# Kernel tuning notes

Measured on AMD Instinct MI355X. Metric: run time of the kernel, lower is better.

Reference implementation:

```python
import jax, jax.numpy as jnp
import numpy as np

EMB = 256   # EMB_SIZE hard-coded in source
H = 8       # num heads (all heads share the same Q/K/V, as in source)
DK = EMB // H  # 32
B, T = 16, 2048
LN_EPS = 1e-5


def _layernorm(a, g, b):
    m = jnp.mean(a, axis=-1, keepdims=True)
    v = jnp.mean(jnp.square(a - m), axis=-1, keepdims=True)
    return (a - m) * jax.lax.rsqrt(v + LN_EPS) * g + b


def setup_inputs() -> dict:
    key = jax.random.key(0)
    ks = jax.random.split(key, 8)
    sc = 0.02
    return {
        "x": jax.random.normal(ks[0], (B, T, EMB), jnp.float32),
        "Wq": jax.random.normal(ks[1], (EMB, DK), jnp.float32) * sc,
        "Wk": jax.random.normal(ks[2], (EMB, DK), jnp.float32) * sc,
        "Wv": jax.random.normal(ks[3], (EMB, DK), jnp.float32) * sc,
        "Wp": jax.random.normal(ks[4], (EMB, EMB), jnp.float32) * sc,
        "bp": jnp.zeros((EMB,), jnp.float32),
        "W1": jax.random.normal(ks[5], (EMB, 4 * EMB), jnp.float32) * sc,
        "b1": jnp.zeros((4 * EMB,), jnp.float32),
        "W2": jax.random.normal(ks[6], (4 * EMB, EMB), jnp.float32) * sc,
        "b2": jnp.zeros((EMB,), jnp.float32),
        "g1": jnp.ones((EMB,), jnp.float32),
        "be1": jnp.zeros((EMB,), jnp.float32),
        "g2": jnp.ones((EMB,), jnp.float32),
        "be2": jnp.zeros((EMB,), jnp.float32),
    }


def reference(x, Wq, Wk, Wv, Wp, bp, W1, b1, W2, b2, g1, be1, g2, be2):
    # Single shared-head QKV projections (bias-free), as in source
    q = x @ Wq  # [B,T,DK]
    k = x @ Wk
    v = x @ Wv
    # Causal self-attention with explicit score matrix [B,T,T]
    scores = jnp.einsum("btd,bsd->bts", q, k) / jnp.sqrt(jnp.float32(DK))
    causal = jnp.tril(jnp.ones((T, T), dtype=bool))
    scores = jnp.where(causal, scores, -jnp.inf)
    a = jax.nn.softmax(scores, axis=-1)
    attn = jnp.einsum("bts,bsd->btd", a, v)  # [B,T,DK]
    # Source concatenates h identical copies of the same attention output
    cat = jnp.tile(attn, (1, 1, H))  # [B,T,EMB]
    mh = cat @ Wp + bp
    y1 = _layernorm(x + mh, g1, be1)
    ff = jax.nn.gelu(y1 @ W1 + b1, approximate=False) @ W2 + b2
    return _layernorm(y1 + ff, g2, be2)
```

## Files before the change

### kernel.cpp

```cpp
#include <hip/hip_runtime.h>

#define BB 16
#define TT 2048
#define EE 256
#define DK 32
#define MM (BB*TT)
#define FF 1024

typedef __bf16 bf16_t;
typedef __bf16 bf16x8 __attribute__((ext_vector_type(8)));
typedef __bf16 bf16x4 __attribute__((ext_vector_type(4)));
typedef float  f32x4  __attribute__((ext_vector_type(4)));

__device__ __forceinline__ f32x4 mfma16(bf16x8 a, bf16x8 b, f32x4 c){
  return __builtin_amdgcn_mfma_f32_16x16x32_bf16(a, b, c, 0, 0, 0);
}
__device__ __forceinline__ void gload_lds16(const void* g, void* l){
  __builtin_amdgcn_global_load_lds((__attribute__((address_space(1))) void*)g,
                                   (__attribute__((address_space(3))) void*)l,
                                   16, 0, 0);
}

__launch_bounds__(256)
__global__ void prep_kernel(const float* __restrict__ Wq, const float* __restrict__ Wk,
                            const float* __restrict__ Wv, const float* __restrict__ Wp,
                            const float* __restrict__ W1, const float* __restrict__ W2,
                            bf16_t* __restrict__ wqkv, float* __restrict__ wpe,
                            bf16_t* __restrict__ w1t, bf16_t* __restrict__ w2t)
{
  const int i = blockIdx.x*256 + threadIdx.x;
  if (i < 96*256) {
    const int r = i >> 8, c = i & 255;
    float v;
    if (r < 32)      v = Wq[c*32 + r] * 0.17677669529663687f;
    else if (r < 64) v = Wk[c*32 + (r-32)];
    else             v = Wv[c*32 + (r-64)];
    wqkv[i] = (bf16_t)v;
  }
  if (i < 32*256) {
    const int d = i >> 8, n = i & 255;
    float s = 0.f;
    #pragma unroll
    for (int h = 0; h < 8; ++h) s += Wp[(h*32 + d)*256 + n];
    wpe[i] = s;
  }
  if (i < 1024*256) {
    const int n = i >> 8, k = i & 255;
    w1t[i] = (bf16_t)W1[(size_t)k*1024 + n];
  }
  if (i < 256*1024) {
    const int n = i >> 10, k = i & 1023;
    w2t[i] = (bf16_t)W2[(size_t)k*256 + n];
  }
}

__launch_bounds__(256)
__global__ void qkv_kernel(const float* __restrict__ x, const bf16_t* __restrict__ wqkv,
                           bf16_t* __restrict__ q, bf16_t* __restrict__ kd,
                           bf16_t* __restrict__ vT)
{
  __shared__ bf16_t Ws[96*256];
  bf16_t* Vt = Ws;
  const int tid = threadIdx.x;
  #pragma unroll
  for (int i = 0; i < 12; ++i) {
    const int v8  = tid + i*256;
    const int row = v8 >> 5;
    const int bir = (v8 & 31) * 16;
    *(bf16x8*)((char*)Ws + row*512 + (bir ^ ((row & 7) << 4))) =
        *(const bf16x8*)(wqkv + (size_t)v8*8);
  }
  __syncthreads();

  const int w = tid >> 6, l = tid & 63;
  const int lr = l & 15, lk4 = l >> 4, lkb = lk4*8;
  const int m0 = blockIdx.x * 64;
  const int arow = m0 + w*16 + lr;
  const float* xr = x + (size_t)arow * 256;

  f32x4 acc[6] = {};
  #pragma unroll
  for (int s = 0; s < 8; ++s) {
    const int kb = s*32 + lkb;
    const float4 v0 = *(const float4*)(xr + kb);
    const float4 v1 = *(const float4*)(xr + kb + 4);
    bf16x8 a;
    a[0]=(bf16_t)v0.x; a[1]=(bf16_t)v0.y; a[2]=(bf16_t)v0.z; a[3]=(bf16_t)v0.w;
    a[4]=(bf16_t)v1.x; a[5]=(bf16_t)v1.y; a[6]=(bf16_t)v1.z; a[7]=(bf16_t)v1.w;
    #pragma unroll
    for (int j = 0; j < 6; ++j) {
      const int nrow = j*16 + lr;
      const bf16x8 bf = *(const bf16x8*)((const char*)Ws + nrow*512 +
                                         ((kb*2) ^ ((nrow & 7) << 4)));
      acc[j] = mfma16(a, bf, acc[j]);
    }
  }
  #pragma unroll
  for (int j = 0; j < 4; ++j) {
    #pragma unroll
    for (int r = 0; r < 4; ++r) {
      const int orow = m0 + w*16 + lk4*4 + r;
      const int col  = j*16 + lr;
      const bf16_t v = (bf16_t)acc[j][r];
      if (col < 32) q[(size_t)orow*32 + col] = v;
      else          kd[(size_t)orow*32 + (col-32)] = v;
    }
  }
  __syncthreads();
  #pragma unroll
  for (int j = 4; j < 6; ++j)
    #pragma unroll
    for (int r = 0; r < 4; ++r) {
      const int d = (j-4)*16 + lr;
      const int t = w*16 + lk4*4 + r;
      *(bf16_t*)((char*)Vt + d*128 + ((((t>>3) ^ (d&7))<<4) | ((t&7)*2))) =
          (bf16_t)acc[j][r];
    }
  __syncthreads();
  {
    const int d = tid >> 3, c8 = tid & 7;
    const bf16x8 v = *(const bf16x8*)((char*)Vt + d*128 + ((c8 ^ (d&7))<<4));
    *(bf16x8*)(vT + ((size_t)(m0 >> 11)*32 + d)*TT + (m0 & 2047) + c8*8) = v;
  }
}

__launch_bounds__(256)
__global__ void attnp_kernel(const bf16_t* __restrict__ q, const bf16_t* __restrict__ kd,
                             const bf16_t* __restrict__ vT,
                             float* __restrict__ part_acc, float* __restrict__ part_ml)
{
  __shared__ bf16_t P[4][16*128];
  const int tid = threadIdx.x;
  const int w = tid >> 6, l = tid & 63;
  const int wv = blockIdx.x*4 + w;
  const int lr = l & 15, g4 = l >> 4;
  const float NEG_INF = -__builtin_inff();

  const int b = wv / 320;
  const int u = wv - b*320;
  int r, base;
  if      (u >= 192) { r = 3; base = 192; }
  else if (u >= 96)  { r = 2; base = 96;  }
  else if (u >= 32)  { r = 1; base = 32;  }
  else               { r = 0; base = 0;   }
  const int qq = u - base;
  const int g  = r*32 + qq / (r+1);
  const int c  = qq - (qq / (r+1))*(r+1);
  const int t_total = (g >> 3) + 1;
  const int t0 = c*4;
  const int t1 = min(t0 + 4, t_total);

  const bf16_t* qb = q  + (size_t)b*TT*32;
  const bf16_t* kb = kd + (size_t)b*TT*32;
  const bf16_t* vb = vT + (size_t)b*32*TT;
  const int q0 = g*16;
  const int qg = q0 + lr;

  const bf16x8 qa = *(const bf16x8*)(qb + (size_t)(q0 + lr)*32 + g4*8);
  const bf16_t* v0r = vb + (size_t)lr*TT;
  const bf16_t* v1r = vb + (size_t)(16 + lr)*TT;

  f32x4 acc0 = {0.f,0.f,0.f,0.f}, acc1 = {0.f,0.f,0.f,0.f};
  float mrun = NEG_INF, lsum = 0.f;
  char* pb = (char*)&P[w][0];
  const int swz = (lr & 7) << 4;
  const f32x4 zf = {0.f,0.f,0.f,0.f};

  for (int t = t0; t < t1; ++t) {
    const int k0 = t * 128;
    f32x4 s[8];
    #pragma unroll
    for (int cc = 0; cc < 8; ++cc) {
      const bf16x8 kf = *(const bf16x8*)(kb + (size_t)(k0 + cc*16 + lr)*32 + g4*8);
      s[cc] = mfma16(kf, qa, zf);
    }
    if (t == t_total - 1) {
      #pragma unroll
      for (int cc = 0; cc < 8; ++cc)
        #pragma unroll
        for (int rr = 0; rr < 4; ++rr)
          if (k0 + cc*16 + g4*4 + rr > qg) s[cc][rr] = NEG_INF;
    }
    float mt = NEG_INF;
    #pragma unroll
    for (int cc = 0; cc < 8; ++cc) {
      float a01 = fmaxf(s[cc][0], s[cc][1]), a23 = fmaxf(s[cc][2], s[cc][3]);
      mt = fmaxf(mt, fmaxf(a01, a23));
    }
    mt = fmaxf(mt, __shfl_xor(mt, 16));
    mt = fmaxf(mt, __shfl_xor(mt, 32));
    const float mn = fmaxf(mrun, mt);
    const float sc = __expf(mrun - mn);
    float ps = 0.f;
    #pragma unroll
    for (int cc = 0; cc < 8; ++cc) {
      float p0 = __expf(s[cc][0]-mn), p1 = __expf(s[cc][1]-mn);
      float p2 = __expf(s[cc][2]-mn), p3 = __expf(s[cc][3]-mn);
      s[cc][0]=p0; s[cc][1]=p1; s[cc][2]=p2; s[cc][3]=p3;
      ps += (p0+p1) + (p2+p3);
    }
    ps += __shfl_xor(ps, 16);
    ps += __shfl_xor(ps, 32);
    lsum = lsum*sc + ps;
    mrun = mn;
    acc0 *= sc; acc1 *= sc;
    #pragma unroll
    for (int cc = 0; cc < 8; ++cc) {
      bf16x4 pk;
      pk[0]=(bf16_t)s[cc][0]; pk[1]=(bf16_t)s[cc][1];
      pk[2]=(bf16_t)s[cc][2]; pk[3]=(bf16_t)s[cc][3];
      *(bf16x4*)(pb + lr*256 + ((cc*32 + g4*8) ^ swz)) = pk;
    }
    #pragma unroll
    for (int h = 0; h < 4; ++h) {
      const bf16x8 pbf = *(const bf16x8*)(pb + lr*256 + ((h*64 + g4*16) ^ swz));
      acc0 = mfma16(*(const bf16x8*)(v0r + k0 + h*32 + g4*8), pbf, acc0);
      acc1 = mfma16(*(const bf16x8*)(v1r + k0 + h*32 + g4*8), pbf, acc1);
    }
  }
  float* pa = part_acc + (size_t)wv*512;
  *(f32x4*)(pa + l*8)     = acc0;
  *(f32x4*)(pa + l*8 + 4) = acc1;
  if (l < 16) {
    part_ml[wv*32 + l]      = mrun;
    part_ml[wv*32 + 16 + l] = lsum;
  }
}

__launch_bounds__(256)
__global__ void attnc_kernel(const float* __restrict__ part_acc,
                             const float* __restrict__ part_ml,
                             bf16_t* __restrict__ attn)
{
  const int tid = threadIdx.x;
  const int id = blockIdx.x*4 + (tid >> 6);
  const int l = tid & 63, lr = l & 15, g4 = l >> 4;
  const int b = id >> 7, g = id & 127;
  const int r = g >> 5;
  const int base = (r == 0) ? 0 : (r == 1) ? 32 : (r == 2) ? 96 : 192;
  const int p0 = b*320 + base + (g - (r << 5))*(r + 1);
  const int nc = r + 1;
  const float NEG_INF = -__builtin_inff();

  float m0v=NEG_INF,m1v=NEG_INF,m2v=NEG_INF,m3v=NEG_INF;
  float l0v=0,l1v=0,l2v=0,l3v=0;
  f32x4 a00={0,0,0,0},a01={0,0,0,0},a10={0,0,0,0},a11={0,0,0,0};
  f32x4 a20={0,0,0,0},a21={0,0,0,0},a30={0,0,0,0},a31={0,0,0,0};
  {
    const float* pa = part_acc + (size_t)p0*512;
    a00 = *(const f32x4*)(pa + l*8); a01 = *(const f32x4*)(pa + l*8 + 4);
    m0v = part_ml[p0*32 + lr]; l0v = part_ml[p0*32 + 16 + lr];
  }
  if (nc > 1) {
    const float* pa = part_acc + (size_t)(p0+1)*512;
    a10 = *(const f32x4*)(pa + l*8); a11 = *(const f32x4*)(pa + l*8 + 4);
    m1v = part_ml[(p0+1)*32 + lr]; l1v = part_ml[(p0+1)*32 + 16 + lr];
  }
  if (nc > 2) {
    const float* pa = part_acc + (size_t)(p0+2)*512;
    a20 = *(const f32x4*)(pa + l*8); a21 = *(const f32x4*)(pa + l*8 + 4);
    m2v = part_ml[(p0+2)*32 + lr]; l2v = part_ml[(p0+2)*32 + 16 + lr];
  }
  if (nc > 3) {
    const float* pa = part_acc + (size_t)(p0+3)*512;
    a30 = *(const f32x4*)(pa + l*8); a31 = *(const f32x4*)(pa + l*8 + 4);
    m3v = part_ml[(p0+3)*32 + lr]; l3v = part_ml[(p0+3)*32 + 16 + lr];
  }
  const float M = fmaxf(fmaxf(m0v, m1v), fmaxf(m2v, m3v));
  const float w0 = __expf(m0v - M), w1 = __expf(m1v - M);
  const float w2 = __expf(m2v - M), w3 = __expf(m3v - M);
  const float L = l0v*w0 + l1v*w1 + l2v*w2 + l3v*w3;
  const float inv = 1.0f / L;
  f32x4 o0 = (a00*w0 + a10*w1 + a20*w2 + a30*w3) * inv;
  f32x4 o1 = (a01*w0 + a11*w1 + a21*w2 + a31*w3) * inv;

  bf16_t* ao = attn + ((size_t)b*TT + g*16 + lr)*32;
  bf16x4 ob0, ob1;
  ob0[0]=(bf16_t)o0[0]; ob0[1]=(bf16_t)o0[1]; ob0[2]=(bf16_t)o0[2]; ob0[3]=(bf16_t)o0[3];
  ob1[0]=(bf16_t)o1[0]; ob1[1]=(bf16_t)o1[1]; ob1[2]=(bf16_t)o1[2]; ob1[3]=(bf16_t)o1[3];
  *(bf16x4*)(ao + g4*4)      = ob0;
  *(bf16x4*)(ao + 16 + g4*4) = ob1;
}

__launch_bounds__(256)
__global__ void ln1_kernel(const float* __restrict__ x, const bf16_t* __restrict__ attn,
                           const float* __restrict__ wpe, const float* __restrict__ bp,
                           const float* __restrict__ g1, const float* __restrict__ be1,
                           bf16_t* __restrict__ y1b)
{
  __shared__ float Wp_s[32*256];
  const int tid = threadIdx.x;
  for (int i = tid; i < 32*64; i += 256)
    ((float4*)Wp_s)[i] = ((const float4*)wpe)[i];
  __syncthreads();

  const int w = tid >> 6, l = tid & 63;
  const int n = l * 4;
  const float4 gv  = *(const float4*)(g1  + n);
  const float4 bev = *(const float4*)(be1 + n);
  const float4 bpv = *(const float4*)(bp  + n);

  #pragma unroll 1
  for (int it = 0; it < 8; ++it) {
    const int row = blockIdx.x*32 + it*4 + w;
    const bf16_t* ar = attn + (size_t)row*32;
    float a[32];
    #pragma unroll
    for (int i = 0; i < 4; ++i) {
      const bf16x8 t = *(const bf16x8*)(ar + i*8);
      #pragma unroll
      for (int j = 0; j < 8; ++j) a[i*8 + j] = (float)t[j];
    }
    float mh[4] = {bpv.x, bpv.y, bpv.z, bpv.w};
    #pragma unroll
    for (int d = 0; d < 32; ++d) {
      const float4 wv = *(const float4*)(Wp_s + d*256 + n);
      const float ad = a[d];
      mh[0] = fmaf(ad, wv.x, mh[0]); mh[1] = fmaf(ad, wv.y, mh[1]);
      mh[2] = fmaf(ad, wv.z, mh[2]); mh[3] = fmaf(ad, wv.w, mh[3]);
    }
    const float4 xv = *(const float4*)(x + (size_t)row*256 + n);
    const float t0 = xv.x + mh[0], t1 = xv.y + mh[1];
    const float t2 = xv.z + mh[2], t3 = xv.w + mh[3];
    float s1 = (t0+t1) + (t2+t3);
    float s2 = (t0*t0 + t1*t1) + (t2*t2 + t3*t3);
    #pragma unroll
    for (int m = 1; m < 64; m <<= 1) { s1 += __shfl_xor(s1, m); s2 += __shfl_xor(s2, m); }
    const float mean = s1 * (1.0f/256.0f);
    const float var  = s2 * (1.0f/256.0f) - mean*mean;
    const float rs   = rsqrtf(var + 1e-5f);
    float4 yv;
    yv.x = (t0-mean)*rs*gv.x + bev.x; yv.y = (t1-mean)*rs*gv.y + bev.y;
    yv.z = (t2-mean)*rs*gv.z + bev.z; yv.w = (t3-mean)*rs*gv.w + bev.w;
    bf16x4 yb; yb[0]=(bf16_t)yv.x; yb[1]=(bf16_t)yv.y; yb[2]=(bf16_t)yv.z; yb[3]=(bf16_t)yv.w;
    *(bf16x4*)(y1b + (size_t)row*256 + n) = yb;
  }
}

__launch_bounds__(256)
__global__ void ff1_kernel(const bf16_t* __restrict__ A, const bf16_t* __restrict__ Bt,
                           const float* __restrict__ b1, bf16_t* __restrict__ H)
{
  __shared__ char SM[32768];
  char* As = SM;
  char* Bs = SM + 16384;
  const int tid = threadIdx.x;
  const int w = tid >> 6, l = tid & 63;
  const int m0 = blockIdx.x * 128, n0 = blockIdx.y * 128;
  const int wm = (w >> 1) * 64, wn = (w & 1) * 64;
  const int lr = l & 15, lk4 = l >> 4;
  const int srow = l >> 3;
  const int scol = ((l & 7) ^ srow) * 8;
  const bf16_t* Ab = A  + (size_t)m0*256 + scol;
  const bf16_t* Bb = Bt + (size_t)n0*256 + scol;

  f32x4 acc[4][4] = {};

  for (int t = 0; t < 4; ++t) {
    const int k0 = t*64;
    #pragma unroll
    for (int i_ = 0; i_ < 4; ++i_) {
      const int r0_ = w*32 + i_*8;
      gload_lds16(Ab + (size_t)(r0_ + srow)*256 + k0, As + r0_*128);
      gload_lds16(Bb + (size_t)(r0_ + srow)*256 + k0, Bs + r0_*128);
    }
    __syncthreads();
    #pragma unroll
    for (int kk = 0; kk < 2; ++kk) {
      bf16x8 af[4], bf[4];
      #pragma unroll
      for (int i = 0; i < 4; ++i) {
        const int row = wm + i*16 + lr;
        af[i] = *(const bf16x8*)(As + row*128 +
                                 ((kk*64 + lk4*16) ^ ((row & 7) << 4)));
      }
      #pragma unroll
      for (int j = 0; j < 4; ++j) {
        const int row = wn + j*16 + lr;
        bf[j] = *(const bf16x8*)(Bs + row*128 +
                                 ((kk*64 + lk4*16) ^ ((row & 7) << 4)));
      }
      #pragma unroll
      for (int i = 0; i < 4; ++i)
        #pragma unroll
        for (int j = 0; j < 4; ++j)
          acc[i][j] = mfma16(af[i], bf[j], acc[i][j]);
    }
    __syncthreads();
  }

  #pragma unroll
  for (int i = 0; i < 4; ++i)
    #pragma unroll
    for (int j = 0; j < 4; ++j) {
      const int col = wn + j*16 + lr;
      const float bias = b1[n0 + col];
      #pragma unroll
      for (int r = 0; r < 4; ++r) {
        const int row = wm + i*16 + lk4*4 + r;
        const float v = acc[i][j][r] + bias;
        const float z = 1.5957691216057308f * v * fmaf(0.044715f, v*v, 1.0f);
        const float gg = v * __builtin_amdgcn_rcpf(1.0f + __expf(-z));
        *(bf16_t*)(SM + row*256 + ((((col>>3) ^ (row&7))<<4) | ((col&7)*2))) =
            (bf16_t)gg;
      }
    }
  __syncthreads();
  #pragma unroll
  for (int p = 0; p < 8; ++p) {
    const int idx = p*256 + tid;
    const int row = idx >> 4, c8 = idx & 15;
    const bf16x8 v = *(const bf16x8*)(SM + row*256 + ((c8 ^ (row&7))<<4));
    *(bf16x8*)(H + (size_t)(m0 + row)*FF + n0 + c8*8) = v;
  }
}

__launch_bounds__(512)
__global__ void ff2_kernel(const bf16_t* __restrict__ A, const bf16_t* __restrict__ Bt,
                           const float* __restrict__ b2, const bf16_t* __restrict__ y1b,
                           const float* __restrict__ g2, const float* __restrict__ be2,
                           float* __restrict__ out)
{
  __shared__ bf16_t As[64*64];
  __shared__ bf16_t Bs[256*64];
  __shared__ float red[64*8];
  const int tid = threadIdx.x;
  const int w = tid >> 6, l = tid & 63;
  const int m0 = blockIdx.x * 64;
  const int wm = (w >> 2) * 32, wn = (w & 3) * 64;
  const int lr = l & 15, lk4 = l >> 4;
  const int srow = l >> 3;
  const int scol = ((l & 7) ^ srow) * 8;
  const bf16_t* Ab = A + (size_t)m0*FF + scol;
  const bf16_t* Bb = Bt + scol;

  f32x4 acc[2][4] = {};

  for (int t = 0; t < 16; ++t) {
    const int k0 = t*64;
    {
      const int r0_ = w*8;
      gload_lds16(Ab + (size_t)(r0_ + srow)*FF + k0, (char*)As + r0_*128);
    }
    #pragma unroll
    for (int i_ = 0; i_ < 4; ++i_) {
      const int r0_ = w*32 + i_*8;
      gload_lds16(Bb + (size_t)(r0_ + srow)*FF + k0, (char*)Bs + r0_*128);
    }
    __syncthreads();
    #pragma unroll
    for (int kk = 0; kk < 2; ++kk) {
      bf16x8 af[2], bf[4];
      #pragma unroll
      for (int i = 0; i < 2; ++i) {
        const int row = wm + i*16 + lr;
        af[i] = *(const bf16x8*)((const char*)As + row*128 +
                                 ((kk*64 + lk4*16) ^ ((row & 7) << 4)));
      }
      #pragma unroll
      for (int j = 0; j < 4; ++j) {
        const int row = wn + j*16 + lr;
        bf[j] = *(const bf16x8*)((const char*)Bs + row*128 +
                                 ((kk*64 + lk4*16) ^ ((row & 7) << 4)));
      }
      #pragma unroll
      for (int i = 0; i < 2; ++i)
        #pragma unroll
        for (int j = 0; j < 4; ++j)
          acc[i][j] = mfma16(af[i], bf[j], acc[i][j]);
    }
    __syncthreads();
  }

  #pragma unroll
  for (int i = 0; i < 2; ++i)
    #pragma unroll
    for (int j = 0; j < 4; ++j) {
      const int col = wn + j*16 + lr;
      #pragma unroll
      for (int r = 0; r < 4; ++r) {
        const int row = m0 + wm + i*16 + lk4*4 + r;
        acc[i][j][r] += b2[col] + (float)y1b[(size_t)row*256 + col];
      }
    }
  #pragma unroll
  for (int i = 0; i < 2; ++i)
    #pragma unroll
    for (int r = 0; r < 4; ++r) {
      float s1 = (acc[i][0][r] + acc[i][1][r]) + (acc[i][2][r] + acc[i][3][r]);
      float s2 = (acc[i][0][r]*acc[i][0][r] + acc[i][1][r]*acc[i][1][r]) +
                 (acc[i][2][r]*acc[i][2][r] + acc[i][3][r]*acc[i][3][r]);
      #pragma unroll
      for (int m = 1; m < 16; m <<= 1) { s1 += __shfl_xor(s1, m); s2 += __shfl_xor(s2, m); }
      if (lr == 0) {
        const int rl = wm + i*16 + lk4*4 + r;
        red[rl*8 + (w & 3)*2]     = s1;
        red[rl*8 + (w & 3)*2 + 1] = s2;
      }
    }
  __syncthreads();
  #pragma unroll
  for (int i = 0; i < 2; ++i)
    #pragma unroll
    for (int r = 0; r < 4; ++r) {
      const int rl = wm + i*16 + lk4*4 + r;
      const float S1 = (red[rl*8+0] + red[rl*8+2]) + (red[rl*8+4] + red[rl*8+6]);
      const float S2 = (red[rl*8+1] + red[rl*8+3]) + (red[rl*8+5] + red[rl*8+7]);
      const float mean = S1 * (1.0f/256.0f);
      const float var  = S2 * (1.0f/256.0f) - mean*mean;
      const float rs   = rsqrtf(var + 1e-5f);
      #pragma unroll
      for (int j = 0; j < 4; ++j) {
        const int col = wn + j*16 + lr;
        out[(size_t)(m0 + rl)*256 + col] = (acc[i][j][r] - mean)*rs*g2[col] + be2[col];
      }
    }
}

extern "C" void kernel_launch(void* const* d_in, const int* in_sizes, int n_in,
                              void* d_out, int out_size, void* d_ws, size_t ws_size,
                              hipStream_t stream)
{
  const float* x   = (const float*)d_in[0];
  const float* Wq  = (const float*)d_in[1];
  const float* Wk  = (const float*)d_in[2];
  const float* Wv  = (const float*)d_in[3];
  const float* Wp  = (const float*)d_in[4];
  const float* bp  = (const float*)d_in[5];
  const float* W1  = (const float*)d_in[6];
  const float* b1  = (const float*)d_in[7];
  const float* W2  = (const float*)d_in[8];
  const float* b2  = (const float*)d_in[9];
  const float* g1  = (const float*)d_in[10];
  const float* be1 = (const float*)d_in[11];
  const float* g2  = (const float*)d_in[12];
  const float* be2 = (const float*)d_in[13];

  char* ws = (char*)d_ws;
  bf16_t* qd   = (bf16_t*)(ws + ((size_t)0  << 20));
  bf16_t* kd   = (bf16_t*)(ws + ((size_t)2  << 20));
  bf16_t* vTd  = (bf16_t*)(ws + ((size_t)4  << 20));
  bf16_t* attn = (bf16_t*)(ws + ((size_t)6  << 20));
  bf16_t* y1b  = (bf16_t*)(ws + ((size_t)8  << 20));
  bf16_t* h1   = (bf16_t*)(ws + ((size_t)24 << 20));
  bf16_t* wqkv = (bf16_t*)(ws + ((size_t)88 << 20));
  float*  wpe  = (float*) (ws + ((size_t)89 << 20));
  bf16_t* w1t  = (bf16_t*)(ws + ((size_t)90 << 20));
  bf16_t* w2t  = (bf16_t*)(ws + ((size_t)91 << 20));
  float*  pml  = (float*) (ws + ((size_t)92 << 20));
  float*  pacc = (float*) (ws + ((size_t)93 << 20));
  float* out = (float*)d_out;

  prep_kernel<<<1024, 256, 0, stream>>>(Wq, Wk, Wv, Wp, W1, W2, wqkv, wpe, w1t, w2t);
  qkv_kernel<<<512, 256, 0, stream>>>(x, wqkv, qd, kd, vTd);
  attnp_kernel<<<1280, 256, 0, stream>>>(qd, kd, vTd, pacc, pml);
  attnc_kernel<<<512, 256, 0, stream>>>(pacc, pml, attn);
  ln1_kernel<<<1024, 256, 0, stream>>>(x, attn, wpe, bp, g1, be1, y1b);
  ff1_kernel<<<dim3(256, 8), 256, 0, stream>>>(y1b, w1t, b1, h1);
  ff2_kernel<<<512, 512, 0, stream>>>(h1, w2t, b2, y1b, g2, be2, out);
}
```

Measured before the change: 147.0 us.

## Double-buffer LDS tiles in FFN GEMM kernels with async global-to-LDS prefetch

Both FFN GEMM kernels (ff1 and ff2) now keep two LDS stages and issue the global-to-LDS loads for tile t+2 while tile t is being computed. Explicit vmcnt waits and raw s_barrier calls replace __syncthreads, and s_setprio raises wave priority during the MFMA section. Bias, gamma and beta values are hoisted into registers before the loop. The cost is more LDS per block (64KB for ff1, 80KB for ff2), which can lower occupancy, and the hand-tuned vmcnt counts must match the number of loads issued per stage.

```diff
diff --git a/kernel.cpp b/kernel.cpp
--- a/kernel.cpp
+++ b/kernel.cpp
@@ -341,9 +341,7 @@
 __global__ void ff1_kernel(const bf16_t* __restrict__ A, const bf16_t* __restrict__ Bt,
                            const float* __restrict__ b1, bf16_t* __restrict__ H)
 {
-  __shared__ char SM[32768];
-  char* As = SM;
-  char* Bs = SM + 16384;
+  __shared__ char SM[65536];
   const int tid = threadIdx.x;
   const int w = tid >> 6, l = tid & 63;
   const int m0 = blockIdx.x * 128, n0 = blockIdx.y * 128;
@@ -354,31 +352,49 @@
   const bf16_t* Ab = A  + (size_t)m0*256 + scol;
   const bf16_t* Bb = Bt + (size_t)n0*256 + scol;
 
+  float bias[4];
+  #pragma unroll
+  for (int j = 0; j < 4; ++j) bias[j] = b1[n0 + wn + j*16 + lr];
+  asm volatile("s_waitcnt vmcnt(0)" ::: "memory");
+  __builtin_amdgcn_sched_barrier(0);
+
+  #define FF1_ST(t, d)                                                        \
+    { const int k0_ = (t)*64;                                                 \
+      _Pragma("unroll")                                                       \
+      for (int i_ = 0; i_ < 4; ++i_) {                                        \
+        const int r0_ = w*32 + i_*8;                                          \
+        gload_lds16(Ab + (size_t)(r0_ + srow)*256 + k0_,                      \
+                    SM + (d)*16384 + r0_*128);                                \
+        gload_lds16(Bb + (size_t)(r0_ + srow)*256 + k0_,                      \
+                    SM + 32768 + (d)*16384 + r0_*128);                        \
+      } }
+
+  FF1_ST(0, 0);
+  FF1_ST(1, 1);
+
   f32x4 acc[4][4] = {};
-
+  #pragma unroll
   for (int t = 0; t < 4; ++t) {
-    const int k0 = t*64;
-    #pragma unroll
-    for (int i_ = 0; i_ < 4; ++i_) {
-      const int r0_ = w*32 + i_*8;
-      gload_lds16(Ab + (size_t)(r0_ + srow)*256 + k0, As + r0_*128);
-      gload_lds16(Bb + (size_t)(r0_ + srow)*256 + k0, Bs + r0_*128);
-    }
-    __syncthreads();
+    if (t < 3) { asm volatile("s_waitcnt vmcnt(8)" ::: "memory"); }
+    else       { asm volatile("s_waitcnt vmcnt(0)" ::: "memory"); }
+    __builtin_amdgcn_sched_barrier(0);
+    __builtin_amdgcn_s_barrier();
+    __builtin_amdgcn_sched_barrier(0);
+    const char* as = SM + (t&1)*16384;
+    const char* bs = SM + 32768 + (t&1)*16384;
+    __builtin_amdgcn_s_setprio(1);
     #pragma unroll
     for (int kk = 0; kk < 2; ++kk) {
       bf16x8 af[4], bf[4];
       #pragma unroll
       for (int i = 0; i < 4; ++i) {
         const int row = wm + i*16 + lr;
-        af[i] = *(const bf16x8*)(As + row*128 +
-                                 ((kk*64 + lk4*16) ^ ((row & 7) << 4)));
+        af[i] = *(const bf16x8*)(as + row*128 + ((kk*64 + lk4*16) ^ ((row & 7) << 4)));
       }
       #pragma unroll
       for (int j = 0; j < 4; ++j) {
         const int row = wn + j*16 + lr;
-        bf[j] = *(const bf16x8*)(Bs + row*128 +
-                                 ((kk*64 + lk4*16) ^ ((row & 7) << 4)));
+        bf[j] = *(const bf16x8*)(bs + row*128 + ((kk*64 + lk4*16) ^ ((row & 7) << 4)));
       }
       #pragma unroll
       for (int i = 0; i < 4; ++i)
@@ -386,19 +402,22 @@
         for (int j = 0; j < 4; ++j)
           acc[i][j] = mfma16(af[i], bf[j], acc[i][j]);
     }
-    __syncthreads();
-  }
+    __builtin_amdgcn_s_setprio(0);
+    __builtin_amdgcn_s_barrier();
+    __builtin_amdgcn_sched_barrier(0);
+    if (t + 2 < 4) FF1_ST(t+2, t&1);
+  }
+  #undef FF1_ST
 
   #pragma unroll
   for (int i = 0; i < 4; ++i)
     #pragma unroll
     for (int j = 0; j < 4; ++j) {
       const int col = wn + j*16 + lr;
-      const float bias = b1[n0 + col];
       #pragma unroll
       for (int r = 0; r < 4; ++r) {
         const int row = wm + i*16 + lk4*4 + r;
-        const float v = acc[i][j][r] + bias;
+        const float v = acc[i][j][r] + bias[j];
         const float z = 1.5957691216057308f * v * fmaf(0.044715f, v*v, 1.0f);
         const float gg = v * __builtin_amdgcn_rcpf(1.0f + __expf(-z));
         *(bf16_t*)(SM + row*256 + ((((col>>3) ^ (row&7))<<4) | ((col&7)*2))) =
@@ -421,9 +440,7 @@
                            const float* __restrict__ g2, const float* __restrict__ be2,
                            float* __restrict__ out)
 {
-  __shared__ bf16_t As[64*64];
-  __shared__ bf16_t Bs[256*64];
-  __shared__ float red[64*8];
+  __shared__ char SM[81920];
   const int tid = threadIdx.x;
   const int w = tid >> 6, l = tid & 63;
   const int m0 = blockIdx.x * 64;
@@ -434,34 +451,52 @@
   const bf16_t* Ab = A + (size_t)m0*FF + scol;
   const bf16_t* Bb = Bt + scol;
 
+  float b2r[4], g2r[4], be2r[4];
+  #pragma unroll
+  for (int j = 0; j < 4; ++j) {
+    const int col = wn + j*16 + lr;
+    b2r[j] = b2[col]; g2r[j] = g2[col]; be2r[j] = be2[col];
+  }
+  asm volatile("s_waitcnt vmcnt(0)" ::: "memory");
+  __builtin_amdgcn_sched_barrier(0);
+
+  #define FF2_ST(t, d)                                                        \
+    { const int k0_ = (t)*64;                                                 \
+      gload_lds16(Ab + (size_t)(w*8 + srow)*FF + k0_,                         \
+                  SM + (d)*8192 + (w*8)*128);                                 \
+      _Pragma("unroll")                                                       \
+      for (int i_ = 0; i_ < 4; ++i_) {                                        \
+        const int r0_ = w*32 + i_*8;                                          \
+        gload_lds16(Bb + (size_t)(r0_ + srow)*FF + k0_,                       \
+                    SM + 16384 + (d)*32768 + r0_*128);                        \
+      } }
+
+  FF2_ST(0, 0);
+  FF2_ST(1, 1);
+
   f32x4 acc[2][4] = {};
-
+  #pragma unroll 1
   for (int t = 0; t < 16; ++t) {
-    const int k0 = t*64;
-    {
-      const int r0_ = w*8;
-      gload_lds16(Ab + (size_t)(r0_ + srow)*FF + k0, (char*)As + r0_*128);
-    }
-    #pragma unroll
-    for (int i_ = 0; i_ < 4; ++i_) {
-      const int r0_ = w*32 + i_*8;
-      gload_lds16(Bb + (size_t)(r0_ + srow)*FF + k0, (char*)Bs + r0_*128);
-    }
-    __syncthreads();
+    if (t < 15) { asm volatile("s_waitcnt vmcnt(5)" ::: "memory"); }
+    else        { asm volatile("s_waitcnt vmcnt(0)" ::: "memory"); }
+    __builtin_amdgcn_sched_barrier(0);
+    __builtin_amdgcn_s_barrier();
+    __builtin_amdgcn_sched_barrier(0);
+    const char* as = SM + (t&1)*8192;
+    const char* bs = SM + 16384 + (t&1)*32768;
+    __builtin_amdgcn_s_setprio(1);
     #pragma unroll
     for (int kk = 0; kk < 2; ++kk) {
       bf16x8 af[2], bf[4];
       #pragma unroll
       for (int i = 0; i < 2; ++i) {
         const int row = wm + i*16 + lr;
-        af[i] = *(const bf16x8*)((const char*)As + row*128 +
-                                 ((kk*64 + lk4*16) ^ ((row & 7) << 4)));
+        af[i] = *(const bf16x8*)(as + row*128 + ((kk*64 + lk4*16) ^ ((row & 7) << 4)));
       }
       #pragma unroll
       for (int j = 0; j < 4; ++j) {
         const int row = wn + j*16 + lr;
-        bf[j] = *(const bf16x8*)((const char*)Bs + row*128 +
-                                 ((kk*64 + lk4*16) ^ ((row & 7) << 4)));
+        bf[j] = *(const bf16x8*)(bs + row*128 + ((kk*64 + lk4*16) ^ ((row & 7) << 4)));
       }
       #pragma unroll
       for (int i = 0; i < 2; ++i)
@@ -469,9 +504,14 @@
         for (int j = 0; j < 4; ++j)
           acc[i][j] = mfma16(af[i], bf[j], acc[i][j]);
     }
-    __syncthreads();
-  }
-
+    __builtin_amdgcn_s_setprio(0);
+    __builtin_amdgcn_s_barrier();
+    __builtin_amdgcn_sched_barrier(0);
+    if (t + 2 < 16) FF2_ST(t+2, t&1);
+  }
+  #undef FF2_ST
+
+  float* red = (float*)SM;
   #pragma unroll
   for (int i = 0; i < 2; ++i)
     #pragma unroll
@@ -480,7 +520,7 @@
       #pragma unroll
       for (int r = 0; r < 4; ++r) {
         const int row = m0 + wm + i*16 + lk4*4 + r;
-        acc[i][j][r] += b2[col] + (float)y1b[(size_t)row*256 + col];
+        acc[i][j][r] += b2r[j] + (float)y1b[(size_t)row*256 + col];
       }
     }
   #pragma unroll
@@ -512,7 +552,7 @@
       #pragma unroll
       for (int j = 0; j < 4; ++j) {
         const int col = wn + j*16 + lr;
-        out[(size_t)(m0 + rl)*256 + col] = (acc[i][j][r] - mean)*rs*g2[col] + be2[col];
+        out[(size_t)(m0 + rl)*256 + col] = (acc[i][j][r] - mean)*rs*g2r[j] + be2r[j];
       }
     }
 }
```

New measurement: 145.3 us. No clear change (-1.2%).
